# Performance work log

Measured on AMD Instinct MI355X. Metric: run time of the kernel, lower is better.

Reference implementation:

```python
import jax, jax.numpy as jnp
import numpy as np

B, S = 8, 1024
D_MODEL = 1024
N_HEAD, HEAD_DIM = 16, 64
FIELD_W, FIELD_H = 32, 32  # S must equal FIELD_W * FIELD_H


def rotate_half(x):
    x1, x2 = jnp.split(x, 2, axis=-1)
    return jnp.concatenate((-x2, x1), axis=-1)


def apply_rope(q, k, cos, sin):
    # q,k: [B,S,H,D]; cos,sin: [S,D] -> broadcast over heads
    c = cos[:, None, :]
    s = sin[:, None, :]
    return q * c + rotate_half(q) * s, k * c + rotate_half(k) * s


def attention(q, k, v):
    # q,k,v: [B,S,H,D]; returns [B,S,H,D]
    scores = jnp.einsum('bqhd,bkhd->bhqk', q, k) * (HEAD_DIM ** -0.5)
    p = jax.nn.softmax(scores, axis=-1)
    return jnp.einsum('bhqk,bkhd->bqhd', p, v)


def setup_inputs() -> dict:
    key = jax.random.key(0)
    ks = jax.random.split(key, 5)
    hidden_states = jax.random.normal(ks[0], (B, S, D_MODEL), jnp.float32)
    cos = jax.random.uniform(ks[1], (S, HEAD_DIM), jnp.float32, minval=-1.0, maxval=1.0)
    sin = jax.random.uniform(ks[2], (S, HEAD_DIM), jnp.float32, minval=-1.0, maxval=1.0)
    w_qkv = jax.random.normal(ks[3], (3 * N_HEAD * HEAD_DIM, D_MODEL), jnp.float32) * (D_MODEL ** -0.5)
    w_o = jax.random.normal(ks[4], (D_MODEL, N_HEAD * HEAD_DIM), jnp.float32) * ((N_HEAD * HEAD_DIM) ** -0.5)
    return {"hidden_states": hidden_states, "cos": cos, "sin": sin, "w_qkv": w_qkv, "w_o": w_o}


def reference(hidden_states, cos, sin, w_qkv, w_o):
    b, s, _ = hidden_states.shape
    qkv = hidden_states @ w_qkv.T                       # [B,S,3*H*D]
    qkv = qkv.reshape(b, s, 3 * N_HEAD, HEAD_DIM)
    q = qkv[:, :, :N_HEAD]
    k = qkv[:, :, N_HEAD:2 * N_HEAD]
    v = qkv[:, :, 2 * N_HEAD:]
    # horizontal pass: standard RoPE
    q1, k1 = apply_rope(q, k, cos[:s], sin[:s])
    attn_out = attention(q1, k1, v)
    # vertical pass: transposed-field RoPE indexing
    idx = jnp.arange(FIELD_W * FIELD_H).reshape(FIELD_W, FIELD_H).T.reshape(-1)
    q2, k2 = apply_rope(q, k, cos[idx], sin[idx])
    attn_out_v = attention(q2, k2, v)
    attn_out = (attn_out + attn_out_v) * 0.5
    return attn_out.reshape(b, s, N_HEAD * HEAD_DIM) @ w_o.T
```

## Files before the change

kernel.cpp:

```cpp
#include <hip/hip_runtime.h>


typedef __attribute__((ext_vector_type(8))) short s16x8;
typedef __attribute__((ext_vector_type(4))) float f32x4;
typedef __attribute__((ext_vector_type(16))) float f32x16;
typedef unsigned short ushort_t;

__device__ __forceinline__ float bf2f(unsigned short u) {
    unsigned x = ((unsigned)u) << 16;
    return __builtin_bit_cast(float, x);
}
__device__ __forceinline__ unsigned short f2bf(float f) {
    unsigned u = __builtin_bit_cast(unsigned, f);
    unsigned r = (u + 0x7fffu + ((u >> 16) & 1u)) >> 16;
    return (unsigned short)r;
}
__device__ __forceinline__ f32x4 mfma16(s16x8 a, s16x8 b, f32x4 c) {
    return __builtin_amdgcn_mfma_f32_16x16x32_bf16(a, b, c, 0, 0, 0);
}
__device__ __forceinline__ f32x16 mfma32(s16x8 a, s16x8 b, f32x16 c) {
    return __builtin_amdgcn_mfma_f32_32x32x16_bf16(a, b, c, 0, 0, 0);
}
__device__ __forceinline__ void gload16(const ushort_t* g, ushort_t* lds) {
    __builtin_amdgcn_global_load_lds(
        (const __attribute__((address_space(1))) unsigned int*)g,
        (__attribute__((address_space(3))) unsigned int*)lds, 16, 0, 0);
}
__device__ __forceinline__ float4 ld4f(const float* p) { return *reinterpret_cast<const float4*>(p); }
__device__ __forceinline__ s16x8 ldg8(const ushort_t* p) { return *reinterpret_cast<const s16x8*>(p); }

__device__ __forceinline__ unsigned cvtpk(float lo, float hi) {
    unsigned r;
    asm("v_cvt_pk_bf16_f32 %0, %1, %2" : "=v"(r) : "v"(lo), "v"(hi));
    return r;
}
__device__ __forceinline__ void pl32swap(unsigned& a, unsigned& b, int hi) {
#if __has_builtin(__builtin_amdgcn_permlane32_swap)
    auto r = __builtin_amdgcn_permlane32_swap((int)a, (int)b, false, false);
    a = (unsigned)r[0]; b = (unsigned)r[1];
#else
    unsigned sa = (unsigned)__shfl_xor((int)a, 32);
    unsigned sb = (unsigned)__shfl_xor((int)b, 32);
    unsigned na = hi ? sb : a;
    unsigned nb = hi ? b : sa;
    a = na; b = nb;
#endif
}
__device__ __forceinline__ s16x8 frag4(unsigned w0, unsigned w1, unsigned w2, unsigned w3) {
    union { unsigned u[4]; s16x8 v; } t;
    t.u[0] = w0; t.u[1] = w1; t.u[2] = w2; t.u[3] = w3;
    return t.v;
}

__global__ __launch_bounds__(256) void conv3(
    const float* __restrict__ sA, ushort_t* __restrict__ dA, int nA,
    const float* __restrict__ sB, ushort_t* __restrict__ dB, int nB,
    const float* __restrict__ sC, ushort_t* __restrict__ dC, int nC)
{
    const int total = nA + nB + nC;
    int i = blockIdx.x * blockDim.x + threadIdx.x;
    const int str = gridDim.x * blockDim.x;
    for (; i < total; i += str) {
        const float* s; ushort_t* d; int off;
        if (i < nA)           { s = sA; d = dA; off = i; }
        else if (i < nA + nB) { s = sB; d = dB; off = i - nA; }
        else                  { s = sC; d = dC; off = i - nA - nB; }
        float4 a = ld4f(s + (size_t)off * 8);
        float4 b = ld4f(s + (size_t)off * 8 + 4);
        s16x8 o;
        o[0] = (short)f2bf(a.x); o[1] = (short)f2bf(a.y); o[2] = (short)f2bf(a.z); o[3] = (short)f2bf(a.w);
        o[4] = (short)f2bf(b.x); o[5] = (short)f2bf(b.y); o[6] = (short)f2bf(b.z); o[7] = (short)f2bf(b.w);
        *reinterpret_cast<s16x8*>(d + (size_t)off * 8) = o;
    }
}

__global__ __launch_bounds__(256) void avg_to_bf16(const float* __restrict__ a,
                                                   const float* __restrict__ b,
                                                   ushort_t* __restrict__ o, int n8)
{
    int i = blockIdx.x * blockDim.x + threadIdx.x;
    const int str = gridDim.x * blockDim.x;
    for (; i < n8; i += str) {
        float4 x0 = ld4f(a + (size_t)i * 8), x1 = ld4f(a + (size_t)i * 8 + 4);
        float4 y0 = ld4f(b + (size_t)i * 8), y1 = ld4f(b + (size_t)i * 8 + 4);
        s16x8 v;
        v[0] = (short)f2bf(0.5f * (x0.x + y0.x)); v[1] = (short)f2bf(0.5f * (x0.y + y0.y));
        v[2] = (short)f2bf(0.5f * (x0.z + y0.z)); v[3] = (short)f2bf(0.5f * (x0.w + y0.w));
        v[4] = (short)f2bf(0.5f * (x1.x + y1.x)); v[5] = (short)f2bf(0.5f * (x1.y + y1.y));
        v[6] = (short)f2bf(0.5f * (x1.z + y1.z)); v[7] = (short)f2bf(0.5f * (x1.w + y1.w));
        *reinterpret_cast<s16x8*>(o + (size_t)i * 8) = v;
    }
}

template<bool SPLIT_QKV>
__global__ __launch_bounds__(256) void gemm_mfma(const ushort_t* __restrict__ A,
                                                 const ushort_t* __restrict__ B,
                                                 void* __restrict__ C0, void* __restrict__ C1,
                                                 void* __restrict__ C2,
                                                 int M, int N, int K)
{
    __shared__ ushort_t As[128 * 64];
    __shared__ ushort_t Bs[128 * 64];
    const int tid = threadIdx.x, l = tid & 63, w = tid >> 6;
    const int lr = l & 15, lg = l >> 4;
    const int m0 = blockIdx.y * 128, n0 = blockIdx.x * 128;
    const int wr = w >> 1, wc = w & 1;

    int srow[4], scol[4];
#pragma unroll
    for (int i = 0; i < 4; ++i) {
        const int chunk = i * 4 + w;
        const int row = chunk * 8 + (l >> 3);
        srow[i] = row;
        scol[i] = ((l & 7) ^ (row & 7)) * 8;
    }

    f32x4 acc[4][4];
#pragma unroll
    for (int mi = 0; mi < 4; ++mi)
#pragma unroll
        for (int ni = 0; ni < 4; ++ni) acc[mi][ni] = (f32x4){0.f, 0.f, 0.f, 0.f};

    for (int k0 = 0; k0 < K; k0 += 64) {
        __syncthreads();
#pragma unroll
        for (int i = 0; i < 4; ++i) {
            gload16(A + (size_t)(m0 + srow[i]) * K + k0 + scol[i], &As[(i * 4 + w) * 512]);
            gload16(B + (size_t)(n0 + srow[i]) * K + k0 + scol[i], &Bs[(i * 4 + w) * 512]);
        }
        __syncthreads();
#pragma unroll
        for (int kf = 0; kf < 2; ++kf) {
            s16x8 af[4], bf[4];
#pragma unroll
            for (int mi = 0; mi < 4; ++mi) {
                const int row = wr * 64 + mi * 16 + lr;
                af[mi] = *reinterpret_cast<const s16x8*>(&As[row * 64 + (((kf * 4 + lg) ^ (row & 7)) << 3)]);
            }
#pragma unroll
            for (int ni = 0; ni < 4; ++ni) {
                const int row = wc * 64 + ni * 16 + lr;
                bf[ni] = *reinterpret_cast<const s16x8*>(&Bs[row * 64 + (((kf * 4 + lg) ^ (row & 7)) << 3)]);
            }
#pragma unroll
            for (int mi = 0; mi < 4; ++mi)
#pragma unroll
                for (int ni = 0; ni < 4; ++ni)
                    acc[mi][ni] = mfma16(af[mi], bf[ni], acc[mi][ni]);
        }
    }

    if (SPLIT_QKV) {
        ushort_t* Cb = (ushort_t*)(n0 < 1024 ? C0 : (n0 < 2048 ? C1 : C2));
        const int nbase = n0 & 1023;
#pragma unroll
        for (int mi = 0; mi < 4; ++mi)
#pragma unroll
            for (int q = 0; q < 4; ++q) {
                const int row = m0 + wr * 64 + mi * 16 + lg * 4 + q;
#pragma unroll
                for (int ni = 0; ni < 4; ++ni)
                    Cb[(size_t)row * 1024 + nbase + wc * 64 + ni * 16 + lr] = f2bf(acc[mi][ni][q]);
            }
    } else {
#pragma unroll
        for (int mi = 0; mi < 4; ++mi)
#pragma unroll
            for (int q = 0; q < 4; ++q) {
                const int row = m0 + wr * 64 + mi * 16 + lg * 4 + q;
#pragma unroll
                for (int ni = 0; ni < 4; ++ni)
                    ((float*)C0)[(size_t)row * N + n0 + wc * 64 + ni * 16 + lr] = acc[mi][ni][q];
            }
    }
}

__global__ __launch_bounds__(256) void rope_rearrange(
    const ushort_t* __restrict__ kb, const ushort_t* __restrict__ vb,
    const float* __restrict__ cosp, const float* __restrict__ sinp,
    ushort_t* __restrict__ Kr, ushort_t* __restrict__ Vt)
{
    __shared__ ushort_t Vs[64 * 65];
    const int tid = threadIdx.x;
    const int sblk = blockIdx.x, h = blockIdx.y, b = blockIdx.z;
    const int r = tid >> 2, c16 = (tid & 3) * 16;
    const int cc = c16 ^ 32;
    const float sg = (c16 < 32) ? -1.f : 1.f;
    const int s = sblk * 64 + r;

    const ushort_t* krow = kb + (size_t)(b * 1024 + s) * 1024 + h * 64;
    const ushort_t* vrow = vb + (size_t)(b * 1024 + s) * 1024 + h * 64;

    s16x8 kx0 = ldg8(krow + c16), kx1 = ldg8(krow + c16 + 8);
    s16x8 ky0 = ldg8(krow + cc),  ky1 = ldg8(krow + cc + 8);

#pragma unroll
    for (int var = 0; var < 2; ++var) {
        const int pos = var ? ((s & 31) * 32 + (s >> 5)) : s;
        const float* crow = cosp + (size_t)pos * 64 + c16;
        const float* srow = sinp + (size_t)pos * 64 + c16;
        ushort_t* kout = Kr + (((size_t)(var * 8 + b) * 16 + h) * 65536)
                            + (size_t)sblk * 4096 + (c16 >> 3) * 512 + r * 8;
        s16x8 o0, o1;
#pragma unroll
        for (int j = 0; j < 8; ++j) {
            o0[j] = (short)f2bf(bf2f((unsigned short)kx0[j]) * crow[j]
                     + sg * bf2f((unsigned short)ky0[j]) * srow[j]);
            o1[j] = (short)f2bf(bf2f((unsigned short)kx1[j]) * crow[j + 8]
                     + sg * bf2f((unsigned short)ky1[j]) * srow[j + 8]);
        }
        *reinterpret_cast<s16x8*>(kout) = o0;
        *reinterpret_cast<s16x8*>(kout + 512) = o1;
    }

    s16x8 v0 = ldg8(vrow + c16), v1 = ldg8(vrow + c16 + 8);
#pragma unroll
    for (int j = 0; j < 8; ++j) {
        Vs[r * 65 + c16 + j] = (ushort_t)v0[j];
        Vs[r * 65 + c16 + 8 + j] = (ushort_t)v1[j];
    }
    __syncthreads();
    {
        const int dd = tid >> 2, cs = (tid & 3) * 16;
        s16x8 t0, t1;
#pragma unroll
        for (int j = 0; j < 8; ++j) {
            t0[j] = (short)Vs[(cs + j) * 65 + dd];
            t1[j] = (short)Vs[(cs + 8 + j) * 65 + dd];
        }
        ushort_t* vout = Vt + ((size_t)(b * 16 + h) * 65536)
                            + (size_t)sblk * 4096 + (cs >> 3) * 512 + dd * 8;
        *reinterpret_cast<s16x8*>(vout) = t0;
        *reinterpret_cast<s16x8*>(vout + 512) = t1;
    }
}

__global__ __launch_bounds__(256) void attn_mfma6(
    const ushort_t* __restrict__ qb,
    const ushort_t* __restrict__ Kr,
    const ushort_t* __restrict__ Vt,
    const float* __restrict__ cosp, const float* __restrict__ sinp,
    float* __restrict__ out0, float* __restrict__ out1)
{
    __shared__ ushort_t Qs[128 * 64];
    __shared__ ushort_t Ks[64 * 64];
    __shared__ ushort_t Vs[64 * 64];

    const int bi = blockIdx.x;
    const int qt = (bi >> 3) & 7;
    const int g = ((bi >> 6) << 3) | (bi & 7);
    const int h = g & 15, bz = g >> 4;
    const int b = bz >> 1, var = bz & 1;

    const int tid = threadIdx.x;
    const int l = tid & 63, wq = tid >> 6;
    const int l31 = l & 31, hi = l >> 5;
    const int s0 = qt * 128;

    {
        const int r = tid >> 1;
        const int half = tid & 1;
        const int c32 = half * 32, cco = 32 - c32;
        const float sg = half ? 1.f : -1.f;
        const int p = s0 + r;
        const int pos = var ? ((p & 31) * 32 + (p >> 5)) : p;
        const ushort_t* qrow = qb + (size_t)(b * 1024 + p) * 1024 + h * 64;
        const float* crow = cosp + (size_t)pos * 64 + c32;
        const float* srow = sinp + (size_t)pos * 64 + c32;
        constexpr float SCALE = 0.125f * 1.44269504f;
#pragma unroll
        for (int u = 0; u < 4; ++u) {
            s16x8 xv = ldg8(qrow + c32 + u * 8);
            s16x8 yv = ldg8(qrow + cco + u * 8);
            s16x8 ov;
#pragma unroll
            for (int j = 0; j < 8; ++j) {
                const int e = u * 8 + j;
                ov[j] = (short)f2bf((bf2f((unsigned short)xv[j]) * crow[e]
                         + sg * bf2f((unsigned short)yv[j]) * srow[e]) * SCALE);
            }
            *reinterpret_cast<s16x8*>(&Qs[((half * 4 + u) * 128 + r) * 8]) = ov;
        }
    }
    __syncthreads();

    s16x8 qf[4];
    {
        const int qrow = wq * 32 + l31;
#pragma unroll
        for (int kc = 0; kc < 4; ++kc)
            qf[kc] = *reinterpret_cast<const s16x8*>(&Qs[((2 * kc + hi) * 128 + qrow) * 8]);
    }

    float l_i = 0.f;
    f32x16 O0, O1;
#pragma unroll
    for (int r = 0; r < 16; ++r) { O0[r] = 0.f; O1[r] = 0.f; }

    const ushort_t* kr_base = Kr + ((size_t)(var * 8 + b) * 16 + h) * 65536;
    const ushort_t* vt_base = Vt + ((size_t)(b * 16 + h)) * 65536;

    for (int kt = 0; kt < 16; ++kt) {
        __syncthreads();
#pragma unroll
        for (int i = 0; i < 2; ++i) {
            const int chunk = wq * 2 + i;
            gload16(kr_base + (size_t)kt * 4096 + chunk * 512 + l * 8, &Ks[chunk * 512]);
            gload16(vt_base + (size_t)kt * 4096 + chunk * 512 + l * 8, &Vs[chunk * 512]);
        }
        __syncthreads();

        f32x16 St0, St1;
#pragma unroll
        for (int r = 0; r < 16; ++r) { St0[r] = 0.f; St1[r] = 0.f; }
#pragma unroll
        for (int kc = 0; kc < 4; ++kc) {
            const int d8 = 2 * kc + hi;
            s16x8 kf0 = *reinterpret_cast<const s16x8*>(&Ks[d8 * 512 + l31 * 8]);
            s16x8 kf1 = *reinterpret_cast<const s16x8*>(&Ks[d8 * 512 + (32 + l31) * 8]);
            St0 = mfma32(kf0, qf[kc], St0);
            St1 = mfma32(kf1, qf[kc], St1);
        }

        float rs0 = 0.f, rs1 = 0.f;
#pragma unroll
        for (int r = 0; r < 16; ++r) { St0[r] = __builtin_amdgcn_exp2f(St0[r]); rs0 += St0[r]; }
#pragma unroll
        for (int r = 0; r < 16; ++r) { St1[r] = __builtin_amdgcn_exp2f(St1[r]); rs1 += St1[r]; }
        l_i += rs0 + rs1;

#pragma unroll
        for (int t = 0; t < 2; ++t) {
            unsigned w0, w1, w2, w3, w4, w5, w6, w7;
            if (t == 0) {
                w0 = cvtpk(St0[0], St0[1]);   w1 = cvtpk(St0[2], St0[3]);
                w2 = cvtpk(St0[4], St0[5]);   w3 = cvtpk(St0[6], St0[7]);
                w4 = cvtpk(St0[8], St0[9]);   w5 = cvtpk(St0[10], St0[11]);
                w6 = cvtpk(St0[12], St0[13]); w7 = cvtpk(St0[14], St0[15]);
            } else {
                w0 = cvtpk(St1[0], St1[1]);   w1 = cvtpk(St1[2], St1[3]);
                w2 = cvtpk(St1[4], St1[5]);   w3 = cvtpk(St1[6], St1[7]);
                w4 = cvtpk(St1[8], St1[9]);   w5 = cvtpk(St1[10], St1[11]);
                w6 = cvtpk(St1[12], St1[13]); w7 = cvtpk(St1[14], St1[15]);
            }
            pl32swap(w0, w2, hi);
            pl32swap(w1, w3, hi);
            pl32swap(w4, w6, hi);
            pl32swap(w5, w7, hi);
            const s16x8 pf0 = frag4(w0, w1, w2, w3);
            const s16x8 pf1 = frag4(w4, w5, w6, w7);
#pragma unroll
            for (int cc = 0; cc < 2; ++cc) {
                const int sg8 = 2 * (2 * t + cc) + hi;
                const s16x8 pf = cc ? pf1 : pf0;
                s16x8 vf0 = *reinterpret_cast<const s16x8*>(&Vs[sg8 * 512 + l31 * 8]);
                s16x8 vf1 = *reinterpret_cast<const s16x8*>(&Vs[sg8 * 512 + (32 + l31) * 8]);
                O0 = mfma32(vf0, pf, O0);
                O1 = mfma32(vf1, pf, O1);
            }
        }
    }

    float* outp = var ? out1 : out0;
    const float inv = 1.f / (l_i + __shfl_xor(l_i, 32));
    const int qrow = s0 + wq * 32 + l31;
    float* orow = outp + (size_t)(b * 1024 + qrow) * 1024 + h * 64;
#pragma unroll
    for (int gq = 0; gq < 4; ++gq) {
        const int d0 = 8 * gq + 4 * hi;
        *reinterpret_cast<float4*>(orow + d0) =
            make_float4(O0[4 * gq] * inv, O0[4 * gq + 1] * inv, O0[4 * gq + 2] * inv, O0[4 * gq + 3] * inv);
        *reinterpret_cast<float4*>(orow + 32 + d0) =
            make_float4(O1[4 * gq] * inv, O1[4 * gq + 1] * inv, O1[4 * gq + 2] * inv, O1[4 * gq + 3] * inv);
    }
}

extern "C" void kernel_launch(void* const* d_in, const int* in_sizes, int n_in,
                              void* d_out, int out_size, void* d_ws, size_t ws_size,
                              hipStream_t stream) {
    const float* hidden = (const float*)d_in[0];
    const float* cosp   = (const float*)d_in[1];
    const float* sinp   = (const float*)d_in[2];
    const float* wqkv   = (const float*)d_in[3];
    const float* wo     = (const float*)d_in[4];
    float* out = (float*)d_out;

    char* wsb = (char*)d_ws;
    ushort_t* hb      = (ushort_t*)(wsb);
    ushort_t* wqkvb   = (ushort_t*)(wsb + (16ull << 20));
    ushort_t* wob     = (ushort_t*)(wsb + (22ull << 20));
    ushort_t* qb      = (ushort_t*)(wsb + (24ull << 20));
    ushort_t* kb      = (ushort_t*)(wsb + (40ull << 20));
    ushort_t* vb      = (ushort_t*)(wsb + (56ull << 20));
    float*    attn0   = (float*)   (wsb + (40ull << 20));
    ushort_t* Kr      = (ushort_t*)(wsb + (72ull << 20));
    ushort_t* Vt      = hb;
    ushort_t* attnavg = (ushort_t*)(wsb + (104ull << 20));

    conv3<<<1536, 256, 0, stream>>>(hidden, hb, 8192 * 1024 / 8,
                                    wqkv, wqkvb, 3072 * 1024 / 8,
                                    wo, wob, 1024 * 1024 / 8);

    gemm_mfma<true><<<dim3(24, 64), 256, 0, stream>>>(hb, wqkvb, qb, kb, vb, 8192, 3072, 1024);

    rope_rearrange<<<dim3(16, 16, 8), 256, 0, stream>>>(kb, vb, cosp, sinp, Kr, Vt);

    attn_mfma6<<<2048, 256, 0, stream>>>(qb, Kr, Vt, cosp, sinp, attn0, out);

    avg_to_bf16<<<2048, 256, 0, stream>>>(attn0, out, attnavg, 8192 * 1024 / 8);

    gemm_mfma<false><<<dim3(8, 64), 256, 0, stream>>>(attnavg, wob, out, nullptr, nullptr, 8192, 1024, 1024);
}
```

Before: 321.6 us.

## Double-buffer K/V tiles in attention kernel and raise MFMA wave priority

Doubles the LDS buffers for the K and V tiles in the attention kernel. The next tile's async global-to-LDS loads are issued before computing on the current tile, and the first tile is prefetched before the Q rope setup. This cuts the two barriers per iteration down to one and overlaps memory latency with MFMA work. It also wraps the QK and PV MFMA sections in s_setprio to favor matrix issue. LDS use per block rises from 32 KB to 48 KB, which may lower the number of resident blocks per CU.

```diff
diff --git a/kernel.cpp b/kernel.cpp
--- a/kernel.cpp
+++ b/kernel.cpp
@@ -235,7 +235,7 @@
     }
 }
 
-__global__ __launch_bounds__(256) void attn_mfma6(
+__global__ __launch_bounds__(256) void attn_mfma7(
     const ushort_t* __restrict__ qb,
     const ushort_t* __restrict__ Kr,
     const ushort_t* __restrict__ Vt,
@@ -243,8 +243,8 @@
     float* __restrict__ out0, float* __restrict__ out1)
 {
     __shared__ ushort_t Qs[128 * 64];
-    __shared__ ushort_t Ks[64 * 64];
-    __shared__ ushort_t Vs[64 * 64];
+    __shared__ ushort_t Ks[2][64 * 64];
+    __shared__ ushort_t Vs[2][64 * 64];
 
     const int bi = blockIdx.x;
     const int qt = (bi >> 3) & 7;
@@ -256,6 +256,16 @@
     const int l = tid & 63, wq = tid >> 6;
     const int l31 = l & 31, hi = l >> 5;
     const int s0 = qt * 128;
+
+    const ushort_t* kr_base = Kr + ((size_t)(var * 8 + b) * 16 + h) * 65536;
+    const ushort_t* vt_base = Vt + ((size_t)(b * 16 + h)) * 65536;
+    const int chunk0 = wq * 2, chunk1 = wq * 2 + 1;
+    const int loff0 = chunk0 * 512 + l * 8, loff1 = chunk1 * 512 + l * 8;
+
+    gload16(kr_base + loff0, &Ks[0][chunk0 * 512]);
+    gload16(kr_base + loff1, &Ks[0][chunk1 * 512]);
+    gload16(vt_base + loff0, &Vs[0][chunk0 * 512]);
+    gload16(vt_base + loff1, &Vs[0][chunk1 * 512]);
 
     {
         const int r = tid >> 1;
@@ -297,30 +307,29 @@
 #pragma unroll
     for (int r = 0; r < 16; ++r) { O0[r] = 0.f; O1[r] = 0.f; }
 
-    const ushort_t* kr_base = Kr + ((size_t)(var * 8 + b) * 16 + h) * 65536;
-    const ushort_t* vt_base = Vt + ((size_t)(b * 16 + h)) * 65536;
-
+    int cur = 0;
     for (int kt = 0; kt < 16; ++kt) {
-        __syncthreads();
-#pragma unroll
-        for (int i = 0; i < 2; ++i) {
-            const int chunk = wq * 2 + i;
-            gload16(kr_base + (size_t)kt * 4096 + chunk * 512 + l * 8, &Ks[chunk * 512]);
-            gload16(vt_base + (size_t)kt * 4096 + chunk * 512 + l * 8, &Vs[chunk * 512]);
-        }
-        __syncthreads();
+        if (kt < 15) {
+            const size_t nb = (size_t)(kt + 1) * 4096;
+            gload16(kr_base + nb + loff0, &Ks[cur ^ 1][chunk0 * 512]);
+            gload16(kr_base + nb + loff1, &Ks[cur ^ 1][chunk1 * 512]);
+            gload16(vt_base + nb + loff0, &Vs[cur ^ 1][chunk0 * 512]);
+            gload16(vt_base + nb + loff1, &Vs[cur ^ 1][chunk1 * 512]);
+        }
 
         f32x16 St0, St1;
 #pragma unroll
         for (int r = 0; r < 16; ++r) { St0[r] = 0.f; St1[r] = 0.f; }
+        __builtin_amdgcn_s_setprio(1);
 #pragma unroll
         for (int kc = 0; kc < 4; ++kc) {
             const int d8 = 2 * kc + hi;
-            s16x8 kf0 = *reinterpret_cast<const s16x8*>(&Ks[d8 * 512 + l31 * 8]);
-            s16x8 kf1 = *reinterpret_cast<const s16x8*>(&Ks[d8 * 512 + (32 + l31) * 8]);
+            s16x8 kf0 = *reinterpret_cast<const s16x8*>(&Ks[cur][d8 * 512 + l31 * 8]);
+            s16x8 kf1 = *reinterpret_cast<const s16x8*>(&Ks[cur][d8 * 512 + (32 + l31) * 8]);
             St0 = mfma32(kf0, qf[kc], St0);
             St1 = mfma32(kf1, qf[kc], St1);
         }
+        __builtin_amdgcn_s_setprio(0);
 
         float rs0 = 0.f, rs1 = 0.f;
 #pragma unroll
@@ -329,6 +338,7 @@
         for (int r = 0; r < 16; ++r) { St1[r] = __builtin_amdgcn_exp2f(St1[r]); rs1 += St1[r]; }
         l_i += rs0 + rs1;
 
+        __builtin_amdgcn_s_setprio(1);
 #pragma unroll
         for (int t = 0; t < 2; ++t) {
             unsigned w0, w1, w2, w3, w4, w5, w6, w7;
@@ -353,12 +363,16 @@
             for (int cc = 0; cc < 2; ++cc) {
                 const int sg8 = 2 * (2 * t + cc) + hi;
                 const s16x8 pf = cc ? pf1 : pf0;
-                s16x8 vf0 = *reinterpret_cast<const s16x8*>(&Vs[sg8 * 512 + l31 * 8]);
-                s16x8 vf1 = *reinterpret_cast<const s16x8*>(&Vs[sg8 * 512 + (32 + l31) * 8]);
+                s16x8 vf0 = *reinterpret_cast<const s16x8*>(&Vs[cur][sg8 * 512 + l31 * 8]);
+                s16x8 vf1 = *reinterpret_cast<const s16x8*>(&Vs[cur][sg8 * 512 + (32 + l31) * 8]);
                 O0 = mfma32(vf0, pf, O0);
                 O1 = mfma32(vf1, pf, O1);
             }
         }
+        __builtin_amdgcn_s_setprio(0);
+
+        __syncthreads();
+        cur ^= 1;
     }
 
     float* outp = var ? out1 : out0;
@@ -405,7 +419,7 @@
 
     rope_rearrange<<<dim3(16, 16, 8), 256, 0, stream>>>(kb, vb, cosp, sinp, Kr, Vt);
 
-    attn_mfma6<<<2048, 256, 0, stream>>>(qb, Kr, Vt, cosp, sinp, attn0, out);
+    attn_mfma7<<<2048, 256, 0, stream>>>(qb, Kr, Vt, cosp, sinp, attn0, out);
 
     avg_to_bf16<<<2048, 256, 0, stream>>>(attn0, out, attnavg, 8192 * 1024 / 8);
 
```

Result: slower. 347.9 us (+8.2%).
